# Performance work log

Measured on AMD Instinct MI355X. Metric: run time of the kernel, lower is better.

## Reference

```python
import jax, jax.numpy as jnp
import numpy as np

N_NODES = 50000
N_EDGES = 800000
IN_NF = 64
OUT_NF = 64
HID = 128
H = 4
D = 64
HD = H * D
EDGE_IN = 2 * IN_NF + 1 + 6   # 135
MSG_IN = HID + 1 + 3 + 6      # 138


def _p(key, i, shape, scale=0.02):
    return scale * jax.random.normal(jax.random.fold_in(key, i), shape, dtype=jnp.float32)


def setup_inputs() -> dict:
    key = jax.random.key(0)
    ks = jax.random.split(key, 4)
    inp = {
        "h": jax.random.normal(ks[0], (N_NODES, IN_NF), dtype=jnp.float32),
        "x": jax.random.normal(ks[1], (N_NODES, 3), dtype=jnp.float32),
        "edge_index": jax.random.randint(ks[2], (2, N_EDGES), 0, N_NODES, dtype=jnp.int32),
        "mask": jnp.ones((N_EDGES,), dtype=bool),
    }
    pk = jax.random.fold_in(key, 7)
    i = iter(range(100))
    inp.update({
        "Wq": _p(pk, next(i), (IN_NF, HD)), "bq": jnp.zeros((HD,)),
        "Wk": _p(pk, next(i), (IN_NF, HD)), "bk": jnp.zeros((HD,)),
        "Wv": _p(pk, next(i), (IN_NF, HD)), "bv": jnp.zeros((HD,)),
        "Wo": _p(pk, next(i), (HD, OUT_NF)), "bo": jnp.zeros((OUT_NF,)),
        "pw1": _p(pk, next(i), (1, HID // 2)), "pb1": jnp.zeros((HID // 2,)),
        "pw2": _p(pk, next(i), (HID // 2, H)), "pb2": jnp.zeros((H,)),
        "ew1": _p(pk, next(i), (EDGE_IN, HID)), "eb1": jnp.zeros((HID,)),
        "ew2": _p(pk, next(i), (HID, HID)), "eb2": jnp.zeros((HID,)),
        "eww": _p(pk, next(i), (HID, H)), "ewb": jnp.zeros((H,)),
        "mw1": _p(pk, next(i), (MSG_IN, HID)), "mb1": jnp.zeros((HID,)),
        "mw2": _p(pk, next(i), (HID, HID)), "mb2": jnp.zeros((HID,)),
        "gw": _p(pk, next(i), (HID, H)), "gb": jnp.zeros((H,)),
        "cw1": _p(pk, next(i), (HID, HID)), "cb1": jnp.zeros((HID,)),
        "cw2": _p(pk, next(i), (HID, H)), "cb2": jnp.zeros((H,)),
        "coord_weights": jnp.ones((H,)),
        "xw1": _p(pk, next(i), (HID, HID)), "xb1": jnp.zeros((HID,)),
        "xw2": _p(pk, next(i), (HID, H)), "xb2": jnp.zeros((H,)),
    })
    return inp


def reference(h, x, edge_index, mask,
              Wq, bq, Wk, bk, Wv, bv, Wo, bo,
              pw1, pb1, pw2, pb2,
              ew1, eb1, ew2, eb2, eww, ewb,
              mw1, mb1, mw2, mb2,
              gw, gb, cw1, cb1, cw2, cb2,
              coord_weights, xw1, xb1, xw2, xb2):
    silu = jax.nn.silu
    row, col = edge_index[0], edge_index[1]
    n = h.shape[0]

    q = (h @ Wq + bq).reshape(n, H, D)
    k = (h @ Wk + bk).reshape(n, H, D)
    v = (h @ Wv + bv).reshape(n, H, D)

    rel_pos = x[row] - x[col]                         # [E,3]
    rel_dist = jnp.sum(rel_pos ** 2, -1, keepdims=True)  # [E,1]
    pos_enc = silu(rel_dist @ pw1 + pb1) @ pw2 + pb2     # [E,H]

    # torch .std() is unbiased (ddof=1)
    xn = (x - x.mean(0, keepdims=True)) / (jnp.std(x, 0, keepdims=True, ddof=1) + 1e-8)

    edge_attr = jnp.concatenate([h[row], h[col], rel_dist, xn[row], xn[col]], -1)
    ef = silu(edge_attr @ ew1 + eb1) @ ew2 + eb2      # [E,HID]
    ewt = ef @ eww + ewb                              # [E,H]

    attn = jnp.einsum('ehd,ehd->eh', q[row], k[col]) / jnp.sqrt(jnp.float32(D))
    attn = attn + pos_enc + ewt
    attn = jnp.where(mask[:, None], attn, jnp.float32(-1e9))

    amax = jax.ops.segment_max(attn, row, num_segments=n)   # [N,H]
    attn = jnp.exp(attn - amax[row])
    asum = jax.ops.segment_sum(attn, row, num_segments=n)
    attn = attn / (asum[row] + 1e-8)                         # [E,H]

    msg_in = jnp.concatenate([ef, attn.mean(1, keepdims=True), rel_pos, xn[row], xn[col]], -1)
    msgs = silu(msg_in @ mw1 + mb1) @ mw2 + mb2              # [E,HID]

    gates = jax.nn.sigmoid(msgs @ gw + gb)                   # [E,H]
    cwts = silu(msgs @ cw1 + cb1) @ cw2 + cb2                # [E,H]

    # per-head index_add into the same buffer == sum over heads of the scalar weight
    s = jnp.sum(gates * cwts * coord_weights, -1, keepdims=True)  # [E,1]
    base = 0.9 * rel_pos + 0.1 * x[col]
    coord_update = jax.ops.segment_sum(s * base / (n - 1), row, num_segments=n)

    cross_v = jnp.cross(rel_pos, jnp.roll(rel_pos, 1, axis=0))
    cg = silu(msgs @ xw1 + xb1) @ xw2 + xb2                  # [E,H]
    cross_s = jnp.sum(cg, -1, keepdims=True)
    coord_update = coord_update + jax.ops.segment_sum(cross_s * cross_v / (n - 1), row, num_segments=n)

    wv = jax.ops.segment_sum(attn[..., None] * v[col], row, num_segments=n)  # [N,H,D]
    out = wv.reshape(n, HD) @ Wo + bo
    return out, coord_update
```

## Files before the change

kernel.cpp:

```cpp
#include <hip/hip_runtime.h>
#include <hip/hip_bf16.h>

#define NN 50000
#define NE 800000

typedef __bf16 bf16x8 __attribute__((ext_vector_type(8)));
typedef float f4v __attribute__((ext_vector_type(4)));

__device__ __forceinline__ float silu_f(float v){
  return v*__builtin_amdgcn_rcpf(1.0f+__expf(-v));
}
__device__ __forceinline__ float bf2f(unsigned int u){ return __uint_as_float(u<<16); }
__device__ __forceinline__ unsigned bfr(float f){
  unsigned b = __float_as_uint(f);
  return b + 0x7fffu + ((b>>16)&1u);
}
__device__ __forceinline__ unsigned short f2bf(float f){ return (unsigned short)(bfr(f)>>16); }
__device__ __forceinline__ unsigned pk2(float a, float b){
  unsigned r;
  asm("v_cvt_pk_bf16_f32 %0, %1, %2" : "=v"(r) : "v"(a), "v"(b));
  return r;
}

union U8 { unsigned short us[8]; uint4 u4; };

__device__ __forceinline__ void pack8(unsigned short* dst, float4 a, float4 b){
  uint4 u;
  u.x = pk2(a.x,a.y); u.y = pk2(a.z,a.w);
  u.z = pk2(b.x,b.y); u.w = pk2(b.z,b.w);
  *(uint4*)dst = u;
}

__device__ __forceinline__ int lidx(int e, int c, int CH){
  return (e*CH + ((c & ~7) | ((c ^ e) & 7))) << 3;
}

template<int KC, int CH>
__device__ __forceinline__ void gemm_rm(const unsigned short* act, const unsigned short* wf,
                                        int wu, int lane, f4v (&acc)[4][2]){
  int le = lane & 15, quad = lane >> 4;
  #pragma unroll
  for (int kc=0;kc<KC;kc++){
    bf16x8 a0 = *(const bf16x8*)(wf + (((wu*2  )*KC + kc)<<9) + lane*8);
    bf16x8 a1 = *(const bf16x8*)(wf + (((wu*2+1)*KC + kc)<<9) + lane*8);
    int chunk = kc*4 + quad;
    #pragma unroll
    for (int et=0;et<4;et++){
      bf16x8 b = *(const bf16x8*)(act + lidx(et*16+le, chunk, CH));
      acc[et][0] = __builtin_amdgcn_mfma_f32_16x16x32_bf16(a0, b, acc[et][0], 0,0,0);
      acc[et][1] = __builtin_amdgcn_mfma_f32_16x16x32_bf16(a1, b, acc[et][1], 0,0,0);
    }
  }
}

template<int CH, bool SILU, bool BIAS>
__device__ __forceinline__ void epi_rm(unsigned short* dst, const f4v (&acc)[4][2],
                                       const float* bias, int wu, int lane){
  int le = lane & 15, quad = lane >> 4;
  #pragma unroll
  for (int ot=0; ot<2; ot++){
    float4 bv = make_float4(0,0,0,0);
    if (BIAS) bv = *(const float4*)(bias + wu*32 + ot*16 + quad*4);
    int chunk = wu*4 + ot*2 + (quad>>1);
    int soff = (quad&1)*4;
    #pragma unroll
    for (int et=0; et<4; et++){
      float v0=acc[et][ot][0], v1=acc[et][ot][1], v2=acc[et][ot][2], v3=acc[et][ot][3];
      if (BIAS){ v0+=bv.x; v1+=bv.y; v2+=bv.z; v3+=bv.w; }
      if (SILU){ v0=silu_f(v0); v1=silu_f(v1); v2=silu_f(v2); v3=silu_f(v3); }
      uint2 u; u.x = pk2(v0,v1); u.y = pk2(v2,v3);
      *(uint2*)(dst + lidx(et*16+le, chunk, CH) + soff) = u;
    }
  }
}

template<int CH>
__device__ __forceinline__ void mfma_head(const unsigned short* buf, const unsigned short* whf,
                                          int wu, int lane, float* dst ){
  int le = lane & 15, quad = lane >> 4;
  f4v hacc = {0.f,0.f,0.f,0.f};
  #pragma unroll
  for (int kc=0;kc<4;kc++){
    bf16x8 a = *(const bf16x8*)(whf + (kc<<9) + lane*8);
    bf16x8 b = *(const bf16x8*)(buf + lidx(wu*16+le, kc*4+quad, CH));
    hacc = __builtin_amdgcn_mfma_f32_16x16x32_bf16(a, b, hacc, 0,0,0);
  }
  if (quad==0){
    #pragma unroll
    for (int r=0;r<4;r++) dst[r*65 + wu*16 + le] = hacc[r];
  }
}

__global__ __launch_bounds__(256) void k_zero(float* __restrict__ p, int n){
  int i = blockIdx.x*256 + threadIdx.x;
  if (i < n) p[i] = 0.f;
}

__global__ __launch_bounds__(256) void k_wcomb(const float* __restrict__ ew2, const float* __restrict__ eww,
                                               const float* __restrict__ eb2, const float* __restrict__ ewb,
                                               const float* __restrict__ pb2,
                                               float* __restrict__ wcomb, float* __restrict__ stats){
  int t = threadIdx.x;
  #pragma unroll
  for (int o=t;o<512;o+=256){
    int i=o>>2, hh=o&3;
    float s=0.f;
    for (int j=0;j<128;j++) s += ew2[i*128+j]*eww[j*4+hh];
    wcomb[o]=s;
  }
  if (t<4){
    float s=0.f;
    for (int j=0;j<128;j++) s += eb2[j]*eww[j*4+t];
    stats[12+t] = s + ewb[t] + pb2[t];
  }
}

__global__ __launch_bounds__(256) void k_wfold(const float* __restrict__ A, const float* __restrict__ Bm,
                                               const float* __restrict__ abias, const float* __restrict__ b2,
                                               float* __restrict__ dstW, float* __restrict__ dstB){
  int idx = blockIdx.x*256 + threadIdx.x;
  if (idx >= 129*128) return;
  int i = idx>>7, n = idx&127;
  if (i<128){
    float s=0.f;
    for (int j=0;j<128;j++) s += A[i*128+j]*Bm[j*128+n];
    dstW[i*128+n]=s;
  } else {
    float s=b2[n];
    for (int j=0;j<128;j++) s += abias[j]*Bm[j*128+n];
    dstB[n]=s;
  }
}

__global__ __launch_bounds__(256) void k_wfoldm(const float* __restrict__ ew2, const float* __restrict__ mw1,
                                                const float* __restrict__ eb2, const float* __restrict__ mb1,
                                                float* __restrict__ dstW, float* __restrict__ dstB){
  int idx = blockIdx.x*256 + threadIdx.x;
  if (idx >= 161*128) return;
  int i = idx>>7, n = idx&127;
  if (i<128){
    float s=0.f;
    for (int j=0;j<128;j++) s += ew2[i*128+j]*mw1[j*128+n];
    dstW[i*128+n]=s;
  } else if (i<160){
    int r = i-144;
    dstW[i*128+n] = (r>=0 && r<10) ? mw1[(128+r)*128+n] : 0.f;
  } else {
    float s=mb1[n];
    for (int j=0;j<128;j++) s += eb2[j]*mw1[j*128+n];
    dstB[n]=s;
  }
}

__global__ __launch_bounds__(256) void k_wfoldg(const float* __restrict__ mw2, const float* __restrict__ gw,
                                                const float* __restrict__ mb2, const float* __restrict__ gb,
                                                float* __restrict__ dstW, float* __restrict__ dstB){
  int idx = blockIdx.x*256 + threadIdx.x;
  if (idx >= 129*4) return;
  int i = idx>>2, hh = idx&3;
  if (i<128){
    float s=0.f;
    for (int j=0;j<128;j++) s += mw2[i*128+j]*gw[j*4+hh];
    dstW[i*4+hh]=s;
  } else {
    float s=gb[hh];
    for (int j=0;j<128;j++) s += mb2[j]*gw[j*4+hh];
    dstB[hh]=s;
  }
}

__global__ __launch_bounds__(256) void k_wprep(const float* __restrict__ src, unsigned short* __restrict__ dst,
                                               int Kreal, int KC){
  int idx = blockIdx.x*256 + threadIdx.x;
  int tot = 8*KC*512;
  if (idx >= tot) return;
  int nt  = idx/(KC*512); int rem = idx%(KC*512);
  int kc  = rem>>9;       int r2  = rem&511;
  int lq  = r2>>3;        int j   = r2&7;
  int k   = kc*32 + (lq>>4)*8 + j;
  int n   = nt*16 + (lq&15);
  float v = (k < Kreal) ? src[k*128 + n] : 0.f;
  dst[idx] = f2bf(v);
}

__global__ __launch_bounds__(256) void k_wprepq(const float* __restrict__ src, unsigned short* __restrict__ dst){
  int idx = blockIdx.x*256 + threadIdx.x;
  if (idx >= 16384) return;
  int nt  = idx>>10;  int rem = idx&1023;
  int kc  = rem>>9;   int r2  = rem&511;
  int lq  = r2>>3;    int j   = r2&7;
  int k   = kc*32 + (lq>>4)*8 + j;
  int n   = nt*16 + (lq&15);
  dst[idx] = f2bf(src[k*256 + n]);
}

__global__ __launch_bounds__(256) void k_wprep4(const float* __restrict__ src, unsigned short* __restrict__ dst){
  int idx = blockIdx.x*256 + threadIdx.x;
  if (idx >= 2048) return;
  int kc = idx>>9; int r2 = idx&511; int lq = r2>>3; int j = r2&7;
  int k = kc*32 + (lq>>4)*8 + j;
  int n = lq&15;
  dst[idx] = f2bf((n<4) ? src[k*4+n] : 0.f);
}

__global__ __launch_bounds__(256) void k_stats(const float* __restrict__ x, float* __restrict__ stats){
  int i = blockIdx.x*256 + threadIdx.x;
  float v0=0.f,v1=0.f,v2=0.f;
  if (i < NN){ v0=x[i*3+0]; v1=x[i*3+1]; v2=x[i*3+2]; }
  float vals[6] = {v0,v1,v2,v0*v0,v1*v1,v2*v2};
  __shared__ float red[256];
  for (int c=0;c<6;c++){
    red[threadIdx.x]=vals[c];
    __syncthreads();
    for (int off=128; off>0; off>>=1){
      if (threadIdx.x < off) red[threadIdx.x] += red[threadIdx.x+off];
      __syncthreads();
    }
    if (threadIdx.x==0) atomicAdd(&stats[c], red[0]);
    __syncthreads();
  }
}

__global__ __launch_bounds__(64) void k_statsfin(float* __restrict__ stats){
  int t = threadIdx.x;
  if (t < 3){
    float s = stats[t], sq = stats[3+t];
    float mean = s/(float)NN;
    float var = (sq - s*s/(float)NN)/(float)(NN-1);
    float sd = sqrtf(var);
    stats[6+t] = mean;
    stats[9+t] = 1.0f/(sd + 1e-8f);
  }
}

__global__ __launch_bounds__(256) void k_qkv2(const float* __restrict__ h,
    const unsigned short* __restrict__ wqf,
    const float* __restrict__ bq, const float* __restrict__ bk, const float* __restrict__ bv,
    unsigned short* __restrict__ q, unsigned short* __restrict__ kk, unsigned short* __restrict__ v){
  __shared__ __align__(16) unsigned short hstage[64*8*8];
  int t = threadIdx.x; int lane = t & 63; int w = t >> 6;
  int wu = __builtin_amdgcn_readfirstlane(w);
  int r0 = blockIdx.x*64;
  {
    int row = r0 + lane;
    float4 a = make_float4(0,0,0,0), b2 = make_float4(0,0,0,0),
           c = make_float4(0,0,0,0), d2 = make_float4(0,0,0,0);
    if (row < NN){
      const float* hr = h + (size_t)row*64 + wu*16;
      a  = *(const float4*)(hr);    b2 = *(const float4*)(hr+4);
      c  = *(const float4*)(hr+8);  d2 = *(const float4*)(hr+12);
    }
    pack8(&hstage[lidx(lane, 2*wu,   8)], a, b2);
    pack8(&hstage[lidx(lane, 2*wu+1, 8)], c, d2);
  }
  __syncthreads();
  int le = lane & 15, quad = lane >> 4;
  #pragma unroll
  for (int ti=0; ti<12; ti++){
    int tt = ti*4 + wu;
    f4v acc[4];
    f4v z = {0.f,0.f,0.f,0.f};
    acc[0]=z; acc[1]=z; acc[2]=z; acc[3]=z;
    #pragma unroll
    for (int kc=0;kc<2;kc++){
      bf16x8 a = *(const bf16x8*)(wqf + ((tt*2 + kc)<<9) + lane*8);
      int chunk = kc*4 + quad;
      #pragma unroll
      for (int et=0;et<4;et++){
        bf16x8 b = *(const bf16x8*)(hstage + lidx(et*16+le, chunk, 8));
        acc[et] = __builtin_amdgcn_mfma_f32_16x16x32_bf16(a, b, acc[et], 0,0,0);
      }
    }
    int mat = tt>>4; int ct = tt&15;
    const float* bias = (mat==0)? bq : (mat==1)? bk : bv;
    unsigned short* outp = (mat==0)? q : (mat==1)? kk : v;
    float4 bv4 = *(const float4*)(bias + ct*16 + quad*4);
    int col = ct*16 + quad*4;
    #pragma unroll
    for (int et=0;et<4;et++){
      int row2 = r0 + et*16 + le;
      if (row2 < NN){
        float v0=acc[et][0]+bv4.x, v1=acc[et][1]+bv4.y, v2=acc[et][2]+bv4.z, v3=acc[et][3]+bv4.w;
        if (mat<2){
          uint2 u; u.x = pk2(v0,v1); u.y = pk2(v2,v3);
          *(uint2*)(outp + (size_t)row2*256 + col) = u;
        } else {
          int head = col>>6, dd = col&63;
          unsigned short* vp = outp + (size_t)row2*256 + (size_t)dd*4 + head;
          vp[0]  = f2bf(v0);
          vp[4]  = f2bf(v1);
          vp[8]  = f2bf(v2);
          vp[12] = f2bf(v3);
        }
      }
    }
  }
}

__global__ __launch_bounds__(256) void k_count(const int* __restrict__ ei, int* __restrict__ counts){
  int e = blockIdx.x*256 + threadIdx.x;
  if (e < NE) atomicAdd(&counts[ei[e]], 1);
}

__global__ __launch_bounds__(256) void k_scan(int* __restrict__ counts, int* __restrict__ offs){
  __shared__ int ps[256];
  int t = threadIdx.x;
  int base = t*196;
  int s = 0;
  for (int i=0;i<196;i++){ int idx = base+i; if (idx < NN) s += counts[idx]; }
  ps[t]=s; __syncthreads();
  for (int off=1; off<256; off<<=1){
    int vv = (t>=off)? ps[t-off] : 0;
    __syncthreads();
    ps[t]+=vv;
    __syncthreads();
  }
  int run = ps[t]-s;
  for (int i=0;i<196;i++){
    int idx = base+i;
    if (idx < NN){ int c = counts[idx]; offs[idx]=run; counts[idx]=run; run+=c; }
  }
  if (t==255) offs[NN]=run;
}

__global__ __launch_bounds__(256) void k_fill(const int* __restrict__ ei, int* __restrict__ cursor, int* __restrict__ elist){
  int e = blockIdx.x*256 + threadIdx.x;
  if (e < NE){
    int r = ei[e];
    int p = atomicAdd(&cursor[r],1);
    elist[p] = e;
  }
}

__global__ __launch_bounds__(256) void k_e1(
    const float* __restrict__ h, const float* __restrict__ x, const int* __restrict__ ei,
    const float* __restrict__ stats,
    const unsigned short* __restrict__ qb, const unsigned short* __restrict__ kb,
    const unsigned short* __restrict__ wfrag, const unsigned short* __restrict__ whfrag,
    const float* __restrict__ eb1,
    const float* __restrict__ pw1, const float* __restrict__ pb1,
    const float* __restrict__ pw2,
    float* __restrict__ asum, float* __restrict__ eattn){
  __shared__ __align__(16) unsigned short bufIn[64*24*8];
  __shared__ float logit_s[256];
  __shared__ float ewt2_s[4*65];
  __shared__ float pos_s[4*65];
  __shared__ float rd_s[64], xnr_s[192], xnc_s[192];
  __shared__ int row_s[64], col_s[64];
  int t = threadIdx.x; int lane = t & 63; int w = t >> 6;
  int wu = __builtin_amdgcn_readfirstlane(w);
  int ebase = blockIdx.x * 64;

  for (int i=t;i<260;i+=256) pos_s[i]=0.f;
  if (t < 64){
    int ge = ebase + t;
    int r = ei[ge], c = ei[NE+ge];
    row_s[t]=r; col_s[t]=c;
    float xr0=x[r*3],xr1=x[r*3+1],xr2=x[r*3+2];
    float xc0=x[c*3],xc1=x[c*3+1],xc2=x[c*3+2];
    float rp0=xr0-xc0, rp1=xr1-xc1, rp2=xr2-xc2;
    rd_s[t]=rp0*rp0+rp1*rp1+rp2*rp2;
    float m0=stats[6],m1=stats[7],m2=stats[8],s0=stats[9],s1=stats[10],s2=stats[11];
    xnr_s[t*3+0]=(xr0-m0)*s0; xnr_s[t*3+1]=(xr1-m1)*s1; xnr_s[t*3+2]=(xr2-m2)*s2;
    xnc_s[t*3+0]=(xc0-m0)*s0; xnc_s[t*3+1]=(xc1-m1)*s1; xnc_s[t*3+2]=(xc2-m2)*s2;
  }
  __syncthreads();

  for (int ii=0; ii<16; ii++){
    int e = wu*16+ii;
    int r = row_s[e], c = col_s[e];
    uint2 qu = *(const uint2*)(qb + (size_t)r*256 + lane*4);
    uint2 ku = *(const uint2*)(kb + (size_t)c*256 + lane*4);
    float d = bf2f(qu.x&0xffffu)*bf2f(ku.x&0xffffu)
            + bf2f(qu.x>>16)   *bf2f(ku.x>>16)
            + bf2f(qu.y&0xffffu)*bf2f(ku.y&0xffffu)
            + bf2f(qu.y>>16)   *bf2f(ku.y>>16);
    d += __shfl_xor(d,1,16); d += __shfl_xor(d,2,16);
    d += __shfl_xor(d,4,16); d += __shfl_xor(d,8,16);
    if ((lane&15)==0) logit_s[e*4 + (lane>>4)] = d*0.125f;
  }
  {
    int jb = wu*16;
    float rd = rd_s[lane];
    float p0=0,p1=0,p2=0,p3=0;
    for (int j=jb; j<jb+16; j++){
      float hp = rd*pw1[j] + pb1[j];
      float hs = silu_f(hp);
      const float4 w4 = *(const float4*)(pw2 + j*4);
      p0+=hs*w4.x; p1+=hs*w4.y; p2+=hs*w4.z; p3+=hs*w4.w;
    }
    atomicAdd(&pos_s[0*65+lane],p0);
    atomicAdd(&pos_s[1*65+lane],p1);
    atomicAdd(&pos_s[2*65+lane],p2);
    atomicAdd(&pos_s[3*65+lane],p3);
  }
  {
    const float* hr = h + (size_t)row_s[lane]*64 + wu*16;
    pack8(&bufIn[lidx(lane, 2*wu,   24)], *(const float4*)(hr),   *(const float4*)(hr+4));
    pack8(&bufIn[lidx(lane, 2*wu+1, 24)], *(const float4*)(hr+8), *(const float4*)(hr+12));
    const float* hc = h + (size_t)col_s[lane]*64 + wu*16;
    pack8(&bufIn[lidx(lane, 8+2*wu, 24)], *(const float4*)(hc),   *(const float4*)(hc+4));
    pack8(&bufIn[lidx(lane, 9+2*wu, 24)], *(const float4*)(hc+8), *(const float4*)(hc+12));
  }
  if (t < 64){
    pack8(&bufIn[lidx(t,16,24)],
          make_float4(rd_s[t], xnr_s[t*3+0], xnr_s[t*3+1], xnr_s[t*3+2]),
          make_float4(xnc_s[t*3+0], xnc_s[t*3+1], xnc_s[t*3+2], 0.f));
  }
  {
    uint4 z4 = make_uint4(0,0,0,0);
    int e = t&63, j = t>>6;
    if (j < 3) *(uint4*)&bufIn[lidx(e, 17+j, 24)] = z4;
  }
  __syncthreads();
  f4v acc[4][2];
  f4v z = {0.f,0.f,0.f,0.f};
  #pragma unroll
  for (int et=0;et<4;et++){ acc[et][0]=z; acc[et][1]=z; }
  gemm_rm<5,24>(bufIn, wfrag + 0, wu, lane, acc);
  __syncthreads();
  epi_rm<24,true,true>(bufIn, acc, eb1, wu, lane);
  __syncthreads();
  mfma_head<24>(bufIn, whfrag + 0, wu, lane, ewt2_s);
  __syncthreads();
  {
    int e2 = t>>2, hh = t&3;
    float lg = logit_s[t] + stats[12+hh] + ewt2_s[hh*65+e2] + pos_s[hh*65+e2];
    float ex = __expf(lg);
    eattn[(size_t)ebase*4 + t] = ex;
    atomicAdd(&asum[row_s[e2]*4 + hh], ex);
  }
}

__global__ __launch_bounds__(256) void k_e2(
    const float* __restrict__ h, const float* __restrict__ x, const int* __restrict__ ei,
    const float* __restrict__ stats,
    const float* __restrict__ asum, const float* __restrict__ eattn,
    const unsigned short* __restrict__ wfrag, const unsigned short* __restrict__ whfrag,
    const float* __restrict__ eb1, const float* __restrict__ fbias,
    const float* __restrict__ cb2, const float* __restrict__ coordw,
    const float* __restrict__ xb2,
    float* __restrict__ cvec){
  __shared__ __align__(16) unsigned short bufIn[64*24*8];
  __shared__ __align__(16) unsigned short bufA [64*16*8];
  __shared__ float g_s[4*65], c_s[4*65], xx_s[4*65];
  __shared__ float s_s[64], cs_s[64];
  __shared__ float rp_s[192], rd_s[64], xnr_s[192], xnc_s[192], xc_s[192];
  __shared__ int row_s[64], col_s[64];
  int t = threadIdx.x; int lane = t & 63; int w = t >> 6;
  int wu = __builtin_amdgcn_readfirstlane(w);
  int ebase = blockIdx.x * 64;

  if (t < 64){
    int ge = ebase + t;
    int r = ei[ge], c = ei[NE+ge];
    row_s[t]=r; col_s[t]=c;
    float xr0=x[r*3],xr1=x[r*3+1],xr2=x[r*3+2];
    float xc0=x[c*3],xc1=x[c*3+1],xc2=x[c*3+2];
    float rp0=xr0-xc0, rp1=xr1-xc1, rp2=xr2-xc2;
    rp_s[t*3+0]=rp0; rp_s[t*3+1]=rp1; rp_s[t*3+2]=rp2;
    rd_s[t]=rp0*rp0+rp1*rp1+rp2*rp2;
    xc_s[t*3+0]=xc0; xc_s[t*3+1]=xc1; xc_s[t*3+2]=xc2;
    float m0=stats[6],m1=stats[7],m2=stats[8],s0=stats[9],s1=stats[10],s2=stats[11];
    xnr_s[t*3+0]=(xr0-m0)*s0; xnr_s[t*3+1]=(xr1-m1)*s1; xnr_s[t*3+2]=(xr2-m2)*s2;
    xnc_s[t*3+0]=(xc0-m0)*s0; xnc_s[t*3+1]=(xc1-m1)*s1; xnc_s[t*3+2]=(xc2-m2)*s2;
  }
  __syncthreads();
  {
    const float* hr = h + (size_t)row_s[lane]*64 + wu*16;
    pack8(&bufIn[lidx(lane, 2*wu,   24)], *(const float4*)(hr),   *(const float4*)(hr+4));
    pack8(&bufIn[lidx(lane, 2*wu+1, 24)], *(const float4*)(hr+8), *(const float4*)(hr+12));
    const float* hc = h + (size_t)col_s[lane]*64 + wu*16;
    pack8(&bufIn[lidx(lane, 8+2*wu, 24)], *(const float4*)(hc),   *(const float4*)(hc+4));
    pack8(&bufIn[lidx(lane, 9+2*wu, 24)], *(const float4*)(hc+8), *(const float4*)(hc+12));
  }
  if (t < 64){
    float4 at = *(const float4*)(eattn + (size_t)(ebase+t)*4);
    const float* as4 = asum + (size_t)row_s[t]*4;
    float am = 0.25f*( at.x/(as4[0]+1e-8f) + at.y/(as4[1]+1e-8f)
                     + at.z/(as4[2]+1e-8f) + at.w/(as4[3]+1e-8f) );
    pack8(&bufIn[lidx(t,16,24)],
          make_float4(rd_s[t], xnr_s[t*3+0], xnr_s[t*3+1], xnr_s[t*3+2]),
          make_float4(xnc_s[t*3+0], xnc_s[t*3+1], xnc_s[t*3+2], 0.f));
    *(uint4*)&bufIn[lidx(t,17,24)] = make_uint4(0,0,0,0);
    pack8(&bufIn[lidx(t,18,24)],
          make_float4(am, rp_s[t*3+0], rp_s[t*3+1], rp_s[t*3+2]),
          make_float4(xnr_s[t*3+0], xnr_s[t*3+1], xnr_s[t*3+2], xnc_s[t*3+0]));
    pack8(&bufIn[lidx(t,19,24)],
          make_float4(xnc_s[t*3+1], xnc_s[t*3+2], 0.f, 0.f),
          make_float4(0.f,0.f,0.f,0.f));
  }
  __syncthreads();
  f4v acc[4][2];
  f4v z = {0.f,0.f,0.f,0.f};
  #pragma unroll
  for (int et=0;et<4;et++){ acc[et][0]=z; acc[et][1]=z; }
  gemm_rm<5,24>(bufIn, wfrag + 0, wu, lane, acc);
  epi_rm<16,true,true>(bufA, acc, eb1, wu, lane);
  __syncthreads();
  #pragma unroll
  for (int et=0;et<4;et++){ acc[et][0]=z; acc[et][1]=z; }
  {
    const unsigned short* wf = wfrag + 20480;
    int le = lane&15, quad = lane>>4;
    #pragma unroll
    for (int kc=0;kc<5;kc++){
      bf16x8 a0 = *(const bf16x8*)(wf + (((wu*2  )*5 + kc)<<9) + lane*8);
      bf16x8 a1 = *(const bf16x8*)(wf + (((wu*2+1)*5 + kc)<<9) + lane*8);
      int chunk = kc*4 + quad;
      #pragma unroll
      for (int et=0;et<4;et++){
        bf16x8 b = (kc<4) ? *(const bf16x8*)(bufA  + lidx(et*16+le, chunk, 16))
                          : *(const bf16x8*)(bufIn + lidx(et*16+le, chunk, 24));
        acc[et][0] = __builtin_amdgcn_mfma_f32_16x16x32_bf16(a0, b, acc[et][0], 0,0,0);
        acc[et][1] = __builtin_amdgcn_mfma_f32_16x16x32_bf16(a1, b, acc[et][1], 0,0,0);
      }
    }
  }
  epi_rm<24,true,true>(bufIn, acc, fbias + 0, wu, lane);
  __syncthreads();
  mfma_head<24>(bufIn, whfrag + 2048, wu, lane, g_s);
  f4v ax[4][2];
  #pragma unroll
  for (int et=0;et<4;et++){ acc[et][0]=z; acc[et][1]=z; ax[et][0]=z; ax[et][1]=z; }
  {
    const unsigned short* wfc = wfrag + 40960;
    const unsigned short* wfx = wfrag + 57344;
    int le = lane&15, quad = lane>>4;
    #pragma unroll
    for (int kc=0;kc<4;kc++){
      bf16x8 ac0 = *(const bf16x8*)(wfc + (((wu*2  )*4 + kc)<<9) + lane*8);
      bf16x8 ac1 = *(const bf16x8*)(wfc + (((wu*2+1)*4 + kc)<<9) + lane*8);
      bf16x8 ax0 = *(const bf16x8*)(wfx + (((wu*2  )*4 + kc)<<9) + lane*8);
      bf16x8 ax1 = *(const bf16x8*)(wfx + (((wu*2+1)*4 + kc)<<9) + lane*8);
      int chunk = kc*4 + quad;
      #pragma unroll
      for (int et=0;et<4;et++){
        bf16x8 b = *(const bf16x8*)(bufIn + lidx(et*16+le, chunk, 24));
        acc[et][0] = __builtin_amdgcn_mfma_f32_16x16x32_bf16(ac0, b, acc[et][0], 0,0,0);
        acc[et][1] = __builtin_amdgcn_mfma_f32_16x16x32_bf16(ac1, b, acc[et][1], 0,0,0);
        ax[et][0]  = __builtin_amdgcn_mfma_f32_16x16x32_bf16(ax0, b, ax[et][0], 0,0,0);
        ax[et][1]  = __builtin_amdgcn_mfma_f32_16x16x32_bf16(ax1, b, ax[et][1], 0,0,0);
      }
    }
  }
  __syncthreads();
  epi_rm<16,true,true>(bufA,  acc, fbias + 128, wu, lane);
  epi_rm<24,true,true>(bufIn, ax,  fbias + 256, wu, lane);
  __syncthreads();
  mfma_head<16>(bufA,  whfrag + 4096, wu, lane, c_s);
  mfma_head<24>(bufIn, whfrag + 6144, wu, lane, xx_s);
  __syncthreads();
  {
    int e2 = t>>2; int hh = t&3;
    float g = __builtin_amdgcn_rcpf(1.0f+__expf(-(g_s[hh*65+e2]+fbias[384+hh])));
    float cwv = c_s[hh*65+e2]+cb2[hh];
    float sv = g*cwv*coordw[hh];
    float csv = xx_s[hh*65+e2]+xb2[hh];
    sv += __shfl_xor(sv,1);  sv += __shfl_xor(sv,2);
    csv += __shfl_xor(csv,1); csv += __shfl_xor(csv,2);
    if (hh==0){ s_s[e2]=sv; cs_s[e2]=csv; }
  }
  __syncthreads();
  if (t < 64){
    int ge = ebase + t;
    float rp0=rp_s[t*3],rp1=rp_s[t*3+1],rp2=rp_s[t*3+2];
    float pp0,pp1,pp2;
    if (t > 0){ pp0=rp_s[(t-1)*3]; pp1=rp_s[(t-1)*3+1]; pp2=rp_s[(t-1)*3+2]; }
    else {
      int gp = (ebase==0)? (NE-1) : (ebase-1);
      int rr=ei[gp], cc2=ei[NE+gp];
      pp0=x[rr*3]-x[cc2*3]; pp1=x[rr*3+1]-x[cc2*3+1]; pp2=x[rr*3+2]-x[cc2*3+2];
    }
    float cv0 = rp1*pp2 - rp2*pp1;
    float cv1 = rp2*pp0 - rp0*pp2;
    float cv2 = rp0*pp1 - rp1*pp0;
    float sv = s_s[t], csv = cs_s[t];
    const float inv = 1.0f/49999.0f;
    cvec[(size_t)ge*3+0] = (sv*(0.9f*rp0+0.1f*xc_s[t*3+0]) + csv*cv0)*inv;
    cvec[(size_t)ge*3+1] = (sv*(0.9f*rp1+0.1f*xc_s[t*3+1]) + csv*cv1)*inv;
    cvec[(size_t)ge*3+2] = (sv*(0.9f*rp2+0.1f*xc_s[t*3+2]) + csv*cv2)*inv;
  }
}

__global__ __launch_bounds__(256) void k_aggout(
    const int* __restrict__ ei, const int* __restrict__ offs, const int* __restrict__ elist,
    const float* __restrict__ eattn, const unsigned short* __restrict__ vb,
    const float* __restrict__ cvec, const float* __restrict__ Wo, const float* __restrict__ bo,
    const float* __restrict__ asum,
    float* __restrict__ outp){
  __shared__ float wvs[4*256];
  int t = threadIdx.x; int lane = t & 63; int w = t >> 6;
  int node = blockIdx.x*4 + w;
  const int* colp = ei + NE;
  int s0 = offs[node], s1 = offs[node+1];
  float a0=0,a1=0,a2=0,a3=0,cc=0;
  int i = s0;
  for (; i+4<=s1; i+=4){
    int e0=elist[i], e1=elist[i+1], e2=elist[i+2], e3=elist[i+3];
    int c0=colp[e0], c1=colp[e1], c2=colp[e2], c3=colp[e3];
    uint2 v0 = *(const uint2*)(vb + (size_t)c0*256 + lane*4);
    uint2 v1 = *(const uint2*)(vb + (size_t)c1*256 + lane*4);
    uint2 v2 = *(const uint2*)(vb + (size_t)c2*256 + lane*4);
    uint2 v3 = *(const uint2*)(vb + (size_t)c3*256 + lane*4);
    float4 at0 = *(const float4*)(eattn + (size_t)e0*4);
    float4 at1 = *(const float4*)(eattn + (size_t)e1*4);
    float4 at2 = *(const float4*)(eattn + (size_t)e2*4);
    float4 at3 = *(const float4*)(eattn + (size_t)e3*4);
    if (lane < 3) cc += cvec[(size_t)e0*3+lane] + cvec[(size_t)e1*3+lane]
                      + cvec[(size_t)e2*3+lane] + cvec[(size_t)e3*3+lane];
    a0 += at0.x*bf2f(v0.x&0xffffu) + at1.x*bf2f(v1.x&0xffffu) + at2.x*bf2f(v2.x&0xffffu) + at3.x*bf2f(v3.x&0xffffu);
    a1 += at0.y*bf2f(v0.x>>16)     + at1.y*bf2f(v1.x>>16)     + at2.y*bf2f(v2.x>>16)     + at3.y*bf2f(v3.x>>16);
    a2 += at0.z*bf2f(v0.y&0xffffu) + at1.z*bf2f(v1.y&0xffffu) + at2.z*bf2f(v2.y&0xffffu) + at3.z*bf2f(v3.y&0xffffu);
    a3 += at0.w*bf2f(v0.y>>16)     + at1.w*bf2f(v1.y>>16)     + at2.w*bf2f(v2.y>>16)     + at3.w*bf2f(v3.y>>16);
  }
  for (; i<s1; i++){
    int e0 = elist[i];
    int c0 = colp[e0];
    uint2 v0 = *(const uint2*)(vb + (size_t)c0*256 + lane*4);
    float4 at0 = *(const float4*)(eattn + (size_t)e0*4);
    if (lane < 3) cc += cvec[(size_t)e0*3+lane];
    a0 += at0.x*bf2f(v0.x&0xffffu);
    a1 += at0.y*bf2f(v0.x>>16);
    a2 += at0.z*bf2f(v0.y&0xffffu);
    a3 += at0.w*bf2f(v0.y>>16);
  }
  {
    const float* as = asum + (size_t)node*4;
    a0 /= (as[0] + 1e-8f);
    a1 /= (as[1] + 1e-8f);
    a2 /= (as[2] + 1e-8f);
    a3 /= (as[3] + 1e-8f);
  }
  wvs[w*256 +       lane]=a0;
  wvs[w*256 +  64 + lane]=a1;
  wvs[w*256 + 128 + lane]=a2;
  wvs[w*256 + 192 + lane]=a3;
  if (lane < 3) outp[(size_t)NN*64 + (size_t)node*3 + lane] = cc;
  float o = bo[lane];
  #pragma unroll 4
  for (int k2=0;k2<256;k2++) o += wvs[w*256+k2] * Wo[k2*64+lane];
  outp[(size_t)node*64 + lane] = o;
}

extern "C" void kernel_launch(void* const* d_in, const int* in_sizes, int n_in,
                              void* d_out, int out_size, void* d_ws, size_t ws_size,
                              hipStream_t stream) {
  const float* h  = (const float*)d_in[0];
  const float* x  = (const float*)d_in[1];
  const int*   ei = (const int*)d_in[2];
  const float* Wq=(const float*)d_in[4];  const float* bq=(const float*)d_in[5];
  const float* Wk=(const float*)d_in[6];  const float* bk=(const float*)d_in[7];
  const float* Wv=(const float*)d_in[8];  const float* bv=(const float*)d_in[9];
  const float* Wo=(const float*)d_in[10]; const float* bo=(const float*)d_in[11];
  const float* pw1=(const float*)d_in[12]; const float* pb1=(const float*)d_in[13];
  const float* pw2=(const float*)d_in[14]; const float* pb2=(const float*)d_in[15];
  const float* ew1=(const float*)d_in[16]; const float* eb1=(const float*)d_in[17];
  const float* ew2=(const float*)d_in[18]; const float* eb2=(const float*)d_in[19];
  const float* eww=(const float*)d_in[20]; const float* ewb=(const float*)d_in[21];
  const float* mw1=(const float*)d_in[22]; const float* mb1=(const float*)d_in[23];
  const float* mw2=(const float*)d_in[24]; const float* mb2=(const float*)d_in[25];
  const float* gw=(const float*)d_in[26];  const float* gb=(const float*)d_in[27];
  const float* cw1=(const float*)d_in[28]; const float* cb1=(const float*)d_in[29];
  const float* cw2=(const float*)d_in[30]; const float* cb2=(const float*)d_in[31];
  const float* coordw=(const float*)d_in[32];
  const float* xw1=(const float*)d_in[33]; const float* xb1=(const float*)d_in[34];
  const float* xw2=(const float*)d_in[35]; const float* xb2=(const float*)d_in[36];

  char* B = (char*)d_ws;
  float* eattn = (float*)(B + 0);
  float* cvec  = (float*)(B + 12800000);
  float* stats = (float*)(B + 22400000);
  float* asum  = (float*)(B + 22400064);
  int* counts  = (int*)(B + 23200064);
  int* offs    = (int*)(B + 23400064);
  unsigned short* wfrag = (unsigned short*)(B + 23600080);
  int* elist   = (int*)(B + 23813088);
  unsigned short* qb = (unsigned short*)(B + 27013088);
  unsigned short* kb = (unsigned short*)(B + 52613088);
  unsigned short* vb = (unsigned short*)(B + 78213088);
  unsigned short* whfrag = (unsigned short*)(B + 103813088);
  float* fbias = (float*)(wfrag + 73728);
  float* wcomb = (float*)elist;
  float* wgf   = wcomb + 512;
  float* wmf   = wgf + 512;
  float* wcf   = wmf + 20608;
  float* wxf   = wcf + 16384;
  unsigned short* qkvf = (unsigned short*)eattn;

  k_zero<<<977,256,0,stream>>>(stats, 250016);
  k_wcomb<<<1,256,0,stream>>>(ew2, eww, eb2, ewb, pb2, wcomb, stats);
  k_wfoldm<<<81,256,0,stream>>>(ew2, mw1, eb2, mb1, wmf, fbias + 0);
  k_wfold<<<65,256,0,stream>>>(mw2, cw1, mb2, cb1, wcf, fbias + 128);
  k_wfold<<<65,256,0,stream>>>(mw2, xw1, mb2, xb1, wxf, fbias + 256);
  k_wfoldg<<<3,256,0,stream>>>(mw2, gw, mb2, gb, wgf, fbias + 384);
  k_wprep<<<80,256,0,stream>>>(ew1, wfrag + 0,     135, 5);
  k_wprep<<<80,256,0,stream>>>(wmf, wfrag + 20480, 160, 5);
  k_wprep<<<64,256,0,stream>>>(wcf, wfrag + 40960, 128, 4);
  k_wprep<<<64,256,0,stream>>>(wxf, wfrag + 57344, 128, 4);
  k_wprepq<<<64,256,0,stream>>>(Wq, qkvf + 0);
  k_wprepq<<<64,256,0,stream>>>(Wk, qkvf + 16384);
  k_wprepq<<<64,256,0,stream>>>(Wv, qkvf + 32768);
  k_wprep4<<<8,256,0,stream>>>(wcomb, whfrag + 0);
  k_wprep4<<<8,256,0,stream>>>(wgf, whfrag + 2048);
  k_wprep4<<<8,256,0,stream>>>(cw2, whfrag + 4096);
  k_wprep4<<<8,256,0,stream>>>(xw2, whfrag + 6144);

  k_stats<<<196,256,0,stream>>>(x, stats);
  k_statsfin<<<1,64,0,stream>>>(stats);
  k_qkv2<<<782,256,0,stream>>>(h, qkvf, bq, bk, bv, qb, kb, vb);
  k_count<<<3125,256,0,stream>>>(ei,counts);
  k_scan<<<1,256,0,stream>>>(counts,offs);
  k_fill<<<3125,256,0,stream>>>(ei,counts,elist);
  k_e1<<<12500,256,0,stream>>>(h,x,ei,stats,qb,kb,wfrag,whfrag,eb1,pw1,pb1,pw2,asum,eattn);
  k_e2<<<12500,256,0,stream>>>(h,x,ei,stats,asum,eattn,wfrag,whfrag,eb1,fbias,cb2,coordw,xb2,cvec);
  k_aggout<<<12500,256,0,stream>>>(ei,offs,elist,eattn,vb,cvec,Wo,bo,asum,(float*)d_out);
}
```

Measured before the change: 1.290 ms.

## Split edge MLP work across 8 waves per block in k_e1 and k_e2

The two edge kernels now launch 512 threads per 64-edge block instead of 256. Each wave computes a 32-output by 32-edge MFMA tile rather than 32 by 64, which halves the per-wave accumulator registers and adds occupancy hints. Gather, logit and positional work are split across the 8 waves, and the head MFMAs are divided between wave groups. In k_e2 the attention-mean loads are also hoisted earlier. In exchange, each weight fragment is loaded twice per block and the extra barriers now span more waves.

```diff
diff --git a/kernel.cpp b/kernel.cpp
--- a/kernel.cpp
+++ b/kernel.cpp
@@ -36,58 +36,58 @@
 }
 
 template<int KC, int CH>
-__device__ __forceinline__ void gemm_rm(const unsigned short* act, const unsigned short* wf,
-                                        int wu, int lane, f4v (&acc)[4][2]){
+__device__ __forceinline__ void gemm8(const unsigned short* act, const unsigned short* wf,
+                                      int q, int eb, int lane, f4v (&acc)[2][2]){
   int le = lane & 15, quad = lane >> 4;
   #pragma unroll
   for (int kc=0;kc<KC;kc++){
-    bf16x8 a0 = *(const bf16x8*)(wf + (((wu*2  )*KC + kc)<<9) + lane*8);
-    bf16x8 a1 = *(const bf16x8*)(wf + (((wu*2+1)*KC + kc)<<9) + lane*8);
+    bf16x8 a0 = *(const bf16x8*)(wf + (((q*2  )*KC + kc)<<9) + lane*8);
+    bf16x8 a1 = *(const bf16x8*)(wf + (((q*2+1)*KC + kc)<<9) + lane*8);
     int chunk = kc*4 + quad;
     #pragma unroll
-    for (int et=0;et<4;et++){
-      bf16x8 b = *(const bf16x8*)(act + lidx(et*16+le, chunk, CH));
-      acc[et][0] = __builtin_amdgcn_mfma_f32_16x16x32_bf16(a0, b, acc[et][0], 0,0,0);
-      acc[et][1] = __builtin_amdgcn_mfma_f32_16x16x32_bf16(a1, b, acc[et][1], 0,0,0);
+    for (int e2=0;e2<2;e2++){
+      bf16x8 b = *(const bf16x8*)(act + lidx((eb+e2)*16+le, chunk, CH));
+      acc[e2][0] = __builtin_amdgcn_mfma_f32_16x16x32_bf16(a0, b, acc[e2][0], 0,0,0);
+      acc[e2][1] = __builtin_amdgcn_mfma_f32_16x16x32_bf16(a1, b, acc[e2][1], 0,0,0);
     }
   }
 }
 
 template<int CH, bool SILU, bool BIAS>
-__device__ __forceinline__ void epi_rm(unsigned short* dst, const f4v (&acc)[4][2],
-                                       const float* bias, int wu, int lane){
+__device__ __forceinline__ void epi8(unsigned short* dst, const f4v (&acc)[2][2],
+                                     const float* bias, int q, int eb, int lane){
   int le = lane & 15, quad = lane >> 4;
   #pragma unroll
   for (int ot=0; ot<2; ot++){
     float4 bv = make_float4(0,0,0,0);
-    if (BIAS) bv = *(const float4*)(bias + wu*32 + ot*16 + quad*4);
-    int chunk = wu*4 + ot*2 + (quad>>1);
+    if (BIAS) bv = *(const float4*)(bias + q*32 + ot*16 + quad*4);
+    int chunk = q*4 + ot*2 + (quad>>1);
     int soff = (quad&1)*4;
     #pragma unroll
-    for (int et=0; et<4; et++){
-      float v0=acc[et][ot][0], v1=acc[et][ot][1], v2=acc[et][ot][2], v3=acc[et][ot][3];
+    for (int e2=0; e2<2; e2++){
+      float v0=acc[e2][ot][0], v1=acc[e2][ot][1], v2=acc[e2][ot][2], v3=acc[e2][ot][3];
       if (BIAS){ v0+=bv.x; v1+=bv.y; v2+=bv.z; v3+=bv.w; }
       if (SILU){ v0=silu_f(v0); v1=silu_f(v1); v2=silu_f(v2); v3=silu_f(v3); }
       uint2 u; u.x = pk2(v0,v1); u.y = pk2(v2,v3);
-      *(uint2*)(dst + lidx(et*16+le, chunk, CH) + soff) = u;
+      *(uint2*)(dst + lidx((eb+e2)*16+le, chunk, CH) + soff) = u;
     }
   }
 }
 
 template<int CH>
 __device__ __forceinline__ void mfma_head(const unsigned short* buf, const unsigned short* whf,
-                                          int wu, int lane, float* dst ){
+                                          int hu, int lane, float* dst ){
   int le = lane & 15, quad = lane >> 4;
   f4v hacc = {0.f,0.f,0.f,0.f};
   #pragma unroll
   for (int kc=0;kc<4;kc++){
     bf16x8 a = *(const bf16x8*)(whf + (kc<<9) + lane*8);
-    bf16x8 b = *(const bf16x8*)(buf + lidx(wu*16+le, kc*4+quad, CH));
+    bf16x8 b = *(const bf16x8*)(buf + lidx(hu*16+le, kc*4+quad, CH));
     hacc = __builtin_amdgcn_mfma_f32_16x16x32_bf16(a, b, hacc, 0,0,0);
   }
   if (quad==0){
     #pragma unroll
-    for (int r=0;r<4;r++) dst[r*65 + wu*16 + le] = hacc[r];
+    for (int r=0;r<4;r++) dst[r*65 + hu*16 + le] = hacc[r];
   }
 }
 
@@ -332,7 +332,7 @@
   }
 }
 
-__global__ __launch_bounds__(256) void k_e1(
+__global__ __launch_bounds__(512, 8) void k_e1(
     const float* __restrict__ h, const float* __restrict__ x, const int* __restrict__ ei,
     const float* __restrict__ stats,
     const unsigned short* __restrict__ qb, const unsigned short* __restrict__ kb,
@@ -349,9 +349,10 @@
   __shared__ int row_s[64], col_s[64];
   int t = threadIdx.x; int lane = t & 63; int w = t >> 6;
   int wu = __builtin_amdgcn_readfirstlane(w);
+  int q = wu & 3, eb = (wu>>2)*2;
   int ebase = blockIdx.x * 64;
 
-  for (int i=t;i<260;i+=256) pos_s[i]=0.f;
+  for (int i=t;i<260;i+=512) pos_s[i]=0.f;
   if (t < 64){
     int ge = ebase + t;
     int r = ei[ge], c = ei[NE+ge];
@@ -366,8 +367,8 @@
   }
   __syncthreads();
 
-  for (int ii=0; ii<16; ii++){
-    int e = wu*16+ii;
+  for (int ii=0; ii<8; ii++){
+    int e = wu*8+ii;
     int r = row_s[e], c = col_s[e];
     uint2 qu = *(const uint2*)(qb + (size_t)r*256 + lane*4);
     uint2 ku = *(const uint2*)(kb + (size_t)c*256 + lane*4);
@@ -380,10 +381,10 @@
     if ((lane&15)==0) logit_s[e*4 + (lane>>4)] = d*0.125f;
   }
   {
-    int jb = wu*16;
+    int jb = wu*8;
     float rd = rd_s[lane];
     float p0=0,p1=0,p2=0,p3=0;
-    for (int j=jb; j<jb+16; j++){
+    for (int j=jb; j<jb+8; j++){
       float hp = rd*pw1[j] + pb1[j];
       float hs = silu_f(hp);
       const float4 w4 = *(const float4*)(pw2 + j*4);
@@ -394,13 +395,15 @@
     atomicAdd(&pos_s[2*65+lane],p2);
     atomicAdd(&pos_s[3*65+lane],p3);
   }
-  {
+  if (wu < 4){
     const float* hr = h + (size_t)row_s[lane]*64 + wu*16;
     pack8(&bufIn[lidx(lane, 2*wu,   24)], *(const float4*)(hr),   *(const float4*)(hr+4));
     pack8(&bufIn[lidx(lane, 2*wu+1, 24)], *(const float4*)(hr+8), *(const float4*)(hr+12));
-    const float* hc = h + (size_t)col_s[lane]*64 + wu*16;
-    pack8(&bufIn[lidx(lane, 8+2*wu, 24)], *(const float4*)(hc),   *(const float4*)(hc+4));
-    pack8(&bufIn[lidx(lane, 9+2*wu, 24)], *(const float4*)(hc+8), *(const float4*)(hc+12));
+  } else {
+    int s = wu-4;
+    const float* hc = h + (size_t)col_s[lane]*64 + s*16;
+    pack8(&bufIn[lidx(lane, 8+2*s, 24)], *(const float4*)(hc),   *(const float4*)(hc+4));
+    pack8(&bufIn[lidx(lane, 9+2*s, 24)], *(const float4*)(hc+8), *(const float4*)(hc+12));
   }
   if (t < 64){
     pack8(&bufIn[lidx(t,16,24)],
@@ -413,17 +416,16 @@
     if (j < 3) *(uint4*)&bufIn[lidx(e, 17+j, 24)] = z4;
   }
   __syncthreads();
-  f4v acc[4][2];
+  f4v acc[2][2];
   f4v z = {0.f,0.f,0.f,0.f};
-  #pragma unroll
-  for (int et=0;et<4;et++){ acc[et][0]=z; acc[et][1]=z; }
-  gemm_rm<5,24>(bufIn, wfrag + 0, wu, lane, acc);
-  __syncthreads();
-  epi_rm<24,true,true>(bufIn, acc, eb1, wu, lane);
-  __syncthreads();
-  mfma_head<24>(bufIn, whfrag + 0, wu, lane, ewt2_s);
-  __syncthreads();
-  {
+  acc[0][0]=z; acc[0][1]=z; acc[1][0]=z; acc[1][1]=z;
+  gemm8<5,24>(bufIn, wfrag + 0, q, eb, lane, acc);
+  __syncthreads();
+  epi8<24,true,true>(bufIn, acc, eb1, q, eb, lane);
+  __syncthreads();
+  if (wu < 4) mfma_head<24>(bufIn, whfrag + 0, wu, lane, ewt2_s);
+  __syncthreads();
+  if (t < 256){
     int e2 = t>>2, hh = t&3;
     float lg = logit_s[t] + stats[12+hh] + ewt2_s[hh*65+e2] + pos_s[hh*65+e2];
     float ex = __expf(lg);
@@ -432,7 +434,7 @@
   }
 }
 
-__global__ __launch_bounds__(256) void k_e2(
+__global__ __launch_bounds__(512, 6) void k_e2(
     const float* __restrict__ h, const float* __restrict__ x, const int* __restrict__ ei,
     const float* __restrict__ stats,
     const float* __restrict__ asum, const float* __restrict__ eattn,
@@ -449,12 +451,17 @@
   __shared__ int row_s[64], col_s[64];
   int t = threadIdx.x; int lane = t & 63; int w = t >> 6;
   int wu = __builtin_amdgcn_readfirstlane(w);
+  int q = wu & 3, eb = (wu>>2)*2;
   int ebase = blockIdx.x * 64;
 
+  float am = 0.f;
   if (t < 64){
     int ge = ebase + t;
     int r = ei[ge], c = ei[NE+ge];
     row_s[t]=r; col_s[t]=c;
+    float4 at = *(const float4*)(eattn + (size_t)ge*4);
+    const float* as4 = asum + (size_t)r*4;
+    float a0=as4[0],a1=as4[1],a2=as4[2],a3=as4[3];
     float xr0=x[r*3],xr1=x[r*3+1],xr2=x[r*3+2];
     float xc0=x[c*3],xc1=x[c*3+1],xc2=x[c*3+2];
     float rp0=xr0-xc0, rp1=xr1-xc1, rp2=xr2-xc2;
@@ -464,21 +471,21 @@
     float m0=stats[6],m1=stats[7],m2=stats[8],s0=stats[9],s1=stats[10],s2=stats[11];
     xnr_s[t*3+0]=(xr0-m0)*s0; xnr_s[t*3+1]=(xr1-m1)*s1; xnr_s[t*3+2]=(xr2-m2)*s2;
     xnc_s[t*3+0]=(xc0-m0)*s0; xnc_s[t*3+1]=(xc1-m1)*s1; xnc_s[t*3+2]=(xc2-m2)*s2;
-  }
-  __syncthreads();
-  {
+    am = 0.25f*( at.x/(a0+1e-8f) + at.y/(a1+1e-8f)
+               + at.z/(a2+1e-8f) + at.w/(a3+1e-8f) );
+  }
+  __syncthreads();
+  if (wu < 4){
     const float* hr = h + (size_t)row_s[lane]*64 + wu*16;
     pack8(&bufIn[lidx(lane, 2*wu,   24)], *(const float4*)(hr),   *(const float4*)(hr+4));
     pack8(&bufIn[lidx(lane, 2*wu+1, 24)], *(const float4*)(hr+8), *(const float4*)(hr+12));
-    const float* hc = h + (size_t)col_s[lane]*64 + wu*16;
-    pack8(&bufIn[lidx(lane, 8+2*wu, 24)], *(const float4*)(hc),   *(const float4*)(hc+4));
-    pack8(&bufIn[lidx(lane, 9+2*wu, 24)], *(const float4*)(hc+8), *(const float4*)(hc+12));
+  } else {
+    int s = wu-4;
+    const float* hc = h + (size_t)col_s[lane]*64 + s*16;
+    pack8(&bufIn[lidx(lane, 8+2*s, 24)], *(const float4*)(hc),   *(const float4*)(hc+4));
+    pack8(&bufIn[lidx(lane, 9+2*s, 24)], *(const float4*)(hc+8), *(const float4*)(hc+12));
   }
   if (t < 64){
-    float4 at = *(const float4*)(eattn + (size_t)(ebase+t)*4);
-    const float* as4 = asum + (size_t)row_s[t]*4;
-    float am = 0.25f*( at.x/(as4[0]+1e-8f) + at.y/(as4[1]+1e-8f)
-                     + at.z/(as4[2]+1e-8f) + at.w/(as4[3]+1e-8f) );
     pack8(&bufIn[lidx(t,16,24)],
           make_float4(rd_s[t], xnr_s[t*3+0], xnr_s[t*3+1], xnr_s[t*3+2]),
           make_float4(xnc_s[t*3+0], xnc_s[t*3+1], xnc_s[t*3+2], 0.f));
@@ -491,67 +498,64 @@
           make_float4(0.f,0.f,0.f,0.f));
   }
   __syncthreads();
-  f4v acc[4][2];
+  f4v acc[2][2], ax[2][2];
   f4v z = {0.f,0.f,0.f,0.f};
-  #pragma unroll
-  for (int et=0;et<4;et++){ acc[et][0]=z; acc[et][1]=z; }
-  gemm_rm<5,24>(bufIn, wfrag + 0, wu, lane, acc);
-  epi_rm<16,true,true>(bufA, acc, eb1, wu, lane);
-  __syncthreads();
-  #pragma unroll
-  for (int et=0;et<4;et++){ acc[et][0]=z; acc[et][1]=z; }
+  acc[0][0]=z; acc[0][1]=z; acc[1][0]=z; acc[1][1]=z;
+  gemm8<5,24>(bufIn, wfrag + 0, q, eb, lane, acc);
+  epi8<16,true,true>(bufA, acc, eb1, q, eb, lane);
+  __syncthreads();
+  acc[0][0]=z; acc[0][1]=z; acc[1][0]=z; acc[1][1]=z;
   {
     const unsigned short* wf = wfrag + 20480;
     int le = lane&15, quad = lane>>4;
     #pragma unroll
     for (int kc=0;kc<5;kc++){
-      bf16x8 a0 = *(const bf16x8*)(wf + (((wu*2  )*5 + kc)<<9) + lane*8);
-      bf16x8 a1 = *(const bf16x8*)(wf + (((wu*2+1)*5 + kc)<<9) + lane*8);
+      bf16x8 a0 = *(const bf16x8*)(wf + (((q*2  )*5 + kc)<<9) + lane*8);
+      bf16x8 a1 = *(const bf16x8*)(wf + (((q*2+1)*5 + kc)<<9) + lane*8);
       int chunk = kc*4 + quad;
       #pragma unroll
-      for (int et=0;et<4;et++){
-        bf16x8 b = (kc<4) ? *(const bf16x8*)(bufA  + lidx(et*16+le, chunk, 16))
-                          : *(const bf16x8*)(bufIn + lidx(et*16+le, chunk, 24));
-        acc[et][0] = __builtin_amdgcn_mfma_f32_16x16x32_bf16(a0, b, acc[et][0], 0,0,0);
-        acc[et][1] = __builtin_amdgcn_mfma_f32_16x16x32_bf16(a1, b, acc[et][1], 0,0,0);
+      for (int e2=0;e2<2;e2++){
+        bf16x8 b = (kc<4) ? *(const bf16x8*)(bufA  + lidx((eb+e2)*16+le, chunk, 16))
+                          : *(const bf16x8*)(bufIn + lidx((eb+e2)*16+le, chunk, 24));
+        acc[e2][0] = __builtin_amdgcn_mfma_f32_16x16x32_bf16(a0, b, acc[e2][0], 0,0,0);
+        acc[e2][1] = __builtin_amdgcn_mfma_f32_16x16x32_bf16(a1, b, acc[e2][1], 0,0,0);
       }
     }
   }
-  epi_rm<24,true,true>(bufIn, acc, fbias + 0, wu, lane);
-  __syncthreads();
-  mfma_head<24>(bufIn, whfrag + 2048, wu, lane, g_s);
-  f4v ax[4][2];
-  #pragma unroll
-  for (int et=0;et<4;et++){ acc[et][0]=z; acc[et][1]=z; ax[et][0]=z; ax[et][1]=z; }
+  epi8<24,true,true>(bufIn, acc, fbias + 0, q, eb, lane);
+  __syncthreads();
+  if (wu < 4) mfma_head<24>(bufIn, whfrag + 2048, wu, lane, g_s);
+  acc[0][0]=z; acc[0][1]=z; acc[1][0]=z; acc[1][1]=z;
+  ax[0][0]=z; ax[0][1]=z; ax[1][0]=z; ax[1][1]=z;
   {
     const unsigned short* wfc = wfrag + 40960;
     const unsigned short* wfx = wfrag + 57344;
     int le = lane&15, quad = lane>>4;
     #pragma unroll
     for (int kc=0;kc<4;kc++){
-      bf16x8 ac0 = *(const bf16x8*)(wfc + (((wu*2  )*4 + kc)<<9) + lane*8);
-      bf16x8 ac1 = *(const bf16x8*)(wfc + (((wu*2+1)*4 + kc)<<9) + lane*8);
-      bf16x8 ax0 = *(const bf16x8*)(wfx + (((wu*2  )*4 + kc)<<9) + lane*8);
-      bf16x8 ax1 = *(const bf16x8*)(wfx + (((wu*2+1)*4 + kc)<<9) + lane*8);
+      bf16x8 ac0 = *(const bf16x8*)(wfc + (((q*2  )*4 + kc)<<9) + lane*8);
+      bf16x8 ac1 = *(const bf16x8*)(wfc + (((q*2+1)*4 + kc)<<9) + lane*8);
+      bf16x8 ax0 = *(const bf16x8*)(wfx + (((q*2  )*4 + kc)<<9) + lane*8);
+      bf16x8 ax1 = *(const bf16x8*)(wfx + (((q*2+1)*4 + kc)<<9) + lane*8);
       int chunk = kc*4 + quad;
       #pragma unroll
-      for (int et=0;et<4;et++){
-        bf16x8 b = *(const bf16x8*)(bufIn + lidx(et*16+le, chunk, 24));
-        acc[et][0] = __builtin_amdgcn_mfma_f32_16x16x32_bf16(ac0, b, acc[et][0], 0,0,0);
-        acc[et][1] = __builtin_amdgcn_mfma_f32_16x16x32_bf16(ac1, b, acc[et][1], 0,0,0);
-        ax[et][0]  = __builtin_amdgcn_mfma_f32_16x16x32_bf16(ax0, b, ax[et][0], 0,0,0);
-        ax[et][1]  = __builtin_amdgcn_mfma_f32_16x16x32_bf16(ax1, b, ax[et][1], 0,0,0);
+      for (int e2=0;e2<2;e2++){
+        bf16x8 b = *(const bf16x8*)(bufIn + lidx((eb+e2)*16+le, chunk, 24));
+        acc[e2][0] = __builtin_amdgcn_mfma_f32_16x16x32_bf16(ac0, b, acc[e2][0], 0,0,0);
+        acc[e2][1] = __builtin_amdgcn_mfma_f32_16x16x32_bf16(ac1, b, acc[e2][1], 0,0,0);
+        ax[e2][0]  = __builtin_amdgcn_mfma_f32_16x16x32_bf16(ax0, b, ax[e2][0], 0,0,0);
+        ax[e2][1]  = __builtin_amdgcn_mfma_f32_16x16x32_bf16(ax1, b, ax[e2][1], 0,0,0);
       }
     }
   }
   __syncthreads();
-  epi_rm<16,true,true>(bufA,  acc, fbias + 128, wu, lane);
-  epi_rm<24,true,true>(bufIn, ax,  fbias + 256, wu, lane);
-  __syncthreads();
-  mfma_head<16>(bufA,  whfrag + 4096, wu, lane, c_s);
-  mfma_head<24>(bufIn, whfrag + 6144, wu, lane, xx_s);
-  __syncthreads();
-  {
+  epi8<16,true,true>(bufA,  acc, fbias + 128, q, eb, lane);
+  epi8<24,true,true>(bufIn, ax,  fbias + 256, q, eb, lane);
+  __syncthreads();
+  if (wu < 4) mfma_head<16>(bufA,  whfrag + 4096, wu,   lane, c_s);
+  else        mfma_head<24>(bufIn, whfrag + 6144, wu-4, lane, xx_s);
+  __syncthreads();
+  if (t < 256){
     int e2 = t>>2; int hh = t&3;
     float g = __builtin_amdgcn_rcpf(1.0f+__expf(-(g_s[hh*65+e2]+fbias[384+hh])));
     float cwv = c_s[hh*65+e2]+cb2[hh];
@@ -712,7 +716,7 @@
   k_count<<<3125,256,0,stream>>>(ei,counts);
   k_scan<<<1,256,0,stream>>>(counts,offs);
   k_fill<<<3125,256,0,stream>>>(ei,counts,elist);
-  k_e1<<<12500,256,0,stream>>>(h,x,ei,stats,qb,kb,wfrag,whfrag,eb1,pw1,pb1,pw2,asum,eattn);
-  k_e2<<<12500,256,0,stream>>>(h,x,ei,stats,asum,eattn,wfrag,whfrag,eb1,fbias,cb2,coordw,xb2,cvec);
+  k_e1<<<12500,512,0,stream>>>(h,x,ei,stats,qb,kb,wfrag,whfrag,eb1,pw1,pb1,pw2,asum,eattn);
+  k_e2<<<12500,512,0,stream>>>(h,x,ei,stats,asum,eattn,wfrag,whfrag,eb1,fbias,cb2,coordw,xb2,cvec);
   k_aggout<<<12500,256,0,stream>>>(ei,offs,elist,eattn,vb,cvec,Wo,bo,asum,(float*)d_out);
 }
```

After: 1.338 ms. 3.7% more time.
